# Performance work log

Measured on AMD Instinct MI355X. Metric: run time of the kernel, lower is better.

## Reference

```python
import jax, jax.numpy as jnp
import numpy as np

TOPK = 4          # config.top_prob_values
NBINS = 32        # config.max_num_bins -> bins per corner = NBINS+1 = 33
HID = 64          # config.lqe_hidden_dim
B, L = 64, 4096


def setup_inputs() -> dict:
    key = jax.random.key(0)
    k1, k2, k3, k4 = jax.random.split(key, 4)
    in_dim = 4 * (TOPK + 1)  # 20
    scores = jax.random.normal(k1, (B, L, 1), dtype=jnp.float32)
    pred_corners = jax.random.normal(k2, (B, L, 4 * (NBINS + 1)), dtype=jnp.float32)
    # Deimv2MLP (DFineMLP) with num_layers=2: Linear(20,64) -> relu -> Linear(64,1)
    w1 = jax.random.normal(k3, (in_dim, HID), dtype=jnp.float32) / np.sqrt(in_dim)
    b1 = jnp.zeros((HID,), dtype=jnp.float32)
    w2 = jax.random.normal(k4, (HID, 1), dtype=jnp.float32) / np.sqrt(HID)
    b2 = jnp.zeros((1,), dtype=jnp.float32)
    return {"scores": scores, "pred_corners": pred_corners,
            "w1": w1, "b1": b1, "w2": w2, "b2": b2}


def reference(scores, pred_corners, w1, b1, w2, b2):
    b, l, _ = pred_corners.shape
    # softmax over bins per corner: (B, L, 4, NBINS+1)
    prob = jax.nn.softmax(pred_corners.reshape(b, l, 4, NBINS + 1), axis=-1)
    prob_topk, _ = jax.lax.top_k(prob, TOPK)                     # (B, L, 4, TOPK)
    stat = jnp.concatenate([prob_topk,
                            prob_topk.mean(axis=-1, keepdims=True)], axis=-1)
    stat = stat.reshape(b, l, 4 * (TOPK + 1))                    # (B, L, 20)
    h = jax.nn.relu(stat @ w1 + b1)                              # (B, L, 64)
    quality_score = h @ w2 + b2                                  # (B, L, 1)
    return scores + quality_score
```

## Files before the change

kernel.cpp:

```cpp
#include <hip/hip_runtime.h>


#define THREADS 256
#define ROWS 64

typedef float f32x4 __attribute__((ext_vector_type(4), aligned(16)));

__device__ __forceinline__ void sort4d(float& a, float& b, float& c, float& d) {
    float t;
    t = fmaxf(a, b); b = fminf(a, b); a = t;
    t = fmaxf(c, d); d = fminf(c, d); c = t;
    t = fmaxf(a, c); c = fminf(a, c); a = t;
    t = fmaxf(b, d); d = fminf(b, d); b = t;
    t = fmaxf(b, c); c = fminf(b, c); b = t;
}
__device__ __forceinline__ void ins4(float& a, float& b, float& c, float& d,
                                     float x) {
    float t;
    t = fmaxf(a, x); x = fminf(a, x); a = t;
    t = fmaxf(b, x); x = fminf(b, x); b = t;
    t = fmaxf(c, x); x = fminf(c, x); c = t;
    d = fmaxf(d, x);
}
__device__ __forceinline__ void merge4(float& a0, float& a1, float& a2,
                                       float& a3, float b0, float b1,
                                       float b2, float b3) {
    a0 = fmaxf(a0, b3);
    a1 = fmaxf(a1, b2);
    a2 = fmaxf(a2, b1);
    a3 = fmaxf(a3, b0);
    sort4d(a0, a1, a2, a3);
}

__global__ __launch_bounds__(THREADS, 4)
void lqe_kernel(const float* __restrict__ scores,
                const float* __restrict__ pc,
                const float* __restrict__ w1,
                const float* __restrict__ b1,
                const float* __restrict__ w2,
                const float* __restrict__ b2,
                float* __restrict__ out)
{
    __shared__ float smStage[ROWS * 132];

    const int t  = threadIdx.x;
    const int wv = t >> 6;
    const int l  = t & 63;
    const long long rowBase = (long long)blockIdx.x * ROWS;

    float sc = 0.f;
    if (t < 64) sc = scores[rowBase + t];

    {
        const f32x4* __restrict__ src =
            (const f32x4*)(pc + rowBase * 132) + wv * 528;
        f32x4* dst = (f32x4*)smStage + wv * 528;
        #pragma unroll
        for (int i = 0; i < 8; ++i) dst[l + i * 64] = src[l + i * 64];
        if (l < 16) dst[512 + l] = src[512 + l];
    }

    {
        const float* v = smStage + wv * 2112 + l * 33;
        float x[33];
        #pragma unroll
        for (int k = 0; k < 33; ++k) x[k] = v[k];

        float a0 = x[0],  a1 = x[1],  a2 = x[2],  a3 = x[3];
        float c0 = x[8],  c1 = x[9],  c2 = x[10], c3 = x[11];
        float d0 = x[16], d1 = x[17], d2 = x[18], d3 = x[19];
        float e0 = x[24], e1 = x[25], e2 = x[26], e3 = x[27];
        sort4d(a0, a1, a2, a3);
        sort4d(c0, c1, c2, c3);
        sort4d(d0, d1, d2, d3);
        sort4d(e0, e1, e2, e3);
        #pragma unroll
        for (int k = 0; k < 4; ++k) {
            ins4(a0, a1, a2, a3, x[4 + k]);
            ins4(c0, c1, c2, c3, x[12 + k]);
            ins4(d0, d1, d2, d3, x[20 + k]);
            ins4(e0, e1, e2, e3, x[28 + k]);
        }
        ins4(e0, e1, e2, e3, x[32]);
        merge4(a0, a1, a2, a3, c0, c1, c2, c3);
        merge4(d0, d1, d2, d3, e0, e1, e2, e3);
        merge4(a0, a1, a2, a3, d0, d1, d2, d3);
        const float t0 = a0, t1 = a1, t2 = a2, t3 = a3;

        float sa = 0.f, sb = 0.f, scc = 0.f, sd = 0.f;
        #pragma unroll
        for (int k = 0; k < 32; k += 4) {
            sa  += __expf(x[k + 0] - t0);
            sb  += __expf(x[k + 1] - t0);
            scc += __expf(x[k + 2] - t0);
            sd  += __expf(x[k + 3] - t0);
        }
        sa += __expf(x[32] - t0);
        const float inv = 1.0f / ((sa + sb) + (scc + sd));
        const float p0 = inv;
        const float p1 = __expf(t1 - t0) * inv;
        const float p2 = __expf(t2 - t0) * inv;
        const float p3 = __expf(t3 - t0) * inv;
        const float pm = 0.25f * (p0 + p1 + p2 + p3);

        float* sd_ = smStage + wv * 2112 + (l >> 2) * 21 + (l & 3) * 5;
        sd_[0] = p0; sd_[1] = p1; sd_[2] = p2; sd_[3] = p3; sd_[4] = pm;
    }
    __syncthreads();

    {
        const int wvs = __builtin_amdgcn_readfirstlane(wv);
        const float* __restrict__ w1s = w1 + wvs * 16;
        const float* __restrict__ w2s = w2 + wvs * 16;
        const float* __restrict__ b1s = b1 + wvs * 16;

        float st[20];
        #pragma unroll
        for (int k = 0; k < 20; ++k)
            st[k] = smStage[(l >> 4) * 2112 + (l & 15) * 21 + k];

        float h[16];
        #pragma unroll
        for (int j = 0; j < 16; ++j) h[j] = b1s[j];
        #pragma unroll
        for (int k = 0; k < 20; ++k) {
            #pragma unroll
            for (int j = 0; j < 16; ++j)
                h[j] = fmaf(st[k], w1s[k * 64 + j], h[j]);
        }
        float acc0 = 0.f, acc1 = 0.f, acc2 = 0.f, acc3 = 0.f;
        #pragma unroll
        for (int j = 0; j < 16; j += 4) {
            acc0 = fmaf(fmaxf(h[j + 0], 0.f), w2s[j + 0], acc0);
            acc1 = fmaf(fmaxf(h[j + 1], 0.f), w2s[j + 1], acc1);
            acc2 = fmaf(fmaxf(h[j + 2], 0.f), w2s[j + 2], acc2);
            acc3 = fmaf(fmaxf(h[j + 3], 0.f), w2s[j + 3], acc3);
        }
        smStage[wvs * 2112 + 400 + l] = (acc0 + acc1) + (acc2 + acc3);
    }
    __syncthreads();

    if (t < 64) {
        const float r = (smStage[400 + t]        + smStage[2112 + 400 + t]) +
                        (smStage[4224 + 400 + t] + smStage[6336 + 400 + t]);
        out[rowBase + t] = sc + r + b2[0];
    }
}

extern "C" void kernel_launch(void* const* d_in, const int* in_sizes, int n_in,
                              void* d_out, int out_size, void* d_ws, size_t ws_size,
                              hipStream_t stream) {
    const float* scores = (const float*)d_in[0];
    const float* pc     = (const float*)d_in[1];
    const float* w1     = (const float*)d_in[2];
    const float* b1     = (const float*)d_in[3];
    const float* w2     = (const float*)d_in[4];
    const float* b2     = (const float*)d_in[5];
    float* out = (float*)d_out;

    const int rows = out_size;
    const int blocks = rows / ROWS;
    lqe_kernel<<<blocks, THREADS, 0, stream>>>(scores, pc, w1, b1, w2, b2, out);
}
```

Before: 33.72 us.

## Process 128 rows per block with both global loads issued before compute

```diff
diff --git a/kernel.cpp b/kernel.cpp
--- a/kernel.cpp
+++ b/kernel.cpp
@@ -2,7 +2,7 @@
 
 
 #define THREADS 256
-#define ROWS 64
+#define BLOCK_ROWS 128
 
 typedef float f32x4 __attribute__((ext_vector_type(4), aligned(16)));
 
@@ -32,7 +32,7 @@
     sort4d(a0, a1, a2, a3);
 }
 
-__global__ __launch_bounds__(THREADS, 4)
+__global__ __launch_bounds__(THREADS, 2)
 void lqe_kernel(const float* __restrict__ scores,
                 const float* __restrict__ pc,
                 const float* __restrict__ w1,
@@ -41,27 +41,33 @@
                 const float* __restrict__ b2,
                 float* __restrict__ out)
 {
-    __shared__ float smStage[ROWS * 132];
+    __shared__ float smStage[BLOCK_ROWS * 132];
 
     const int t  = threadIdx.x;
     const int wv = t >> 6;
     const int l  = t & 63;
-    const long long rowBase = (long long)blockIdx.x * ROWS;
+    const long long rowBase = (long long)blockIdx.x * BLOCK_ROWS;
 
     float sc = 0.f;
-    if (t < 64) sc = scores[rowBase + t];
+    if (t < BLOCK_ROWS) sc = scores[rowBase + t];
 
-    {
+    const int g0 = 2 * wv, g1 = 2 * wv + 1;
+
+    auto load_g = [&](int g, f32x4 (&r)[8], f32x4& tl) {
         const f32x4* __restrict__ src =
-            (const f32x4*)(pc + rowBase * 132) + wv * 528;
-        f32x4* dst = (f32x4*)smStage + wv * 528;
+            (const f32x4*)(pc + (rowBase + (long long)g * 16) * 132);
         #pragma unroll
-        for (int i = 0; i < 8; ++i) dst[l + i * 64] = src[l + i * 64];
-        if (l < 16) dst[512 + l] = src[512 + l];
-    }
-
-    {
-        const float* v = smStage + wv * 2112 + l * 33;
+        for (int i = 0; i < 8; ++i) r[i] = src[l + i * 64];
+        if (l < 16) tl = src[512 + l];
+    };
+    auto write_g = [&](int g, const f32x4 (&r)[8], const f32x4& tl) {
+        f32x4* dst = (f32x4*)smStage + g * 528;
+        #pragma unroll
+        for (int i = 0; i < 8; ++i) dst[l + i * 64] = r[i];
+        if (l < 16) dst[512 + l] = tl;
+    };
+    auto corner_g = [&](int g) {
+        const float* v = smStage + g * 2112 + l * 33;
         float x[33];
         #pragma unroll
         for (int k = 0; k < 33; ++k) x[k] = v[k];
@@ -103,9 +109,17 @@
         const float p3 = __expf(t3 - t0) * inv;
         const float pm = 0.25f * (p0 + p1 + p2 + p3);
 
-        float* sd_ = smStage + wv * 2112 + (l >> 2) * 21 + (l & 3) * 5;
+        float* sd_ = smStage + g * 2112 + (l >> 2) * 21 + (l & 3) * 5;
         sd_[0] = p0; sd_[1] = p1; sd_[2] = p2; sd_[3] = p3; sd_[4] = pm;
-    }
+    };
+
+    f32x4 ra[8], rb[8], ta, tb;
+    load_g(g0, ra, ta);
+    load_g(g1, rb, tb);
+    write_g(g0, ra, ta);
+    corner_g(g0);
+    write_g(g1, rb, tb);
+    corner_g(g1);
     __syncthreads();
 
     {
@@ -114,35 +128,39 @@
         const float* __restrict__ w2s = w2 + wvs * 16;
         const float* __restrict__ b1s = b1 + wvs * 16;
 
-        float st[20];
         #pragma unroll
-        for (int k = 0; k < 20; ++k)
-            st[k] = smStage[(l >> 4) * 2112 + (l & 15) * 21 + k];
+        for (int half = 0; half < 2; ++half) {
+            const int r = half * 64 + l;
+            float st[20];
+            #pragma unroll
+            for (int k = 0; k < 20; ++k)
+                st[k] = smStage[(r >> 4) * 2112 + (r & 15) * 21 + k];
 
-        float h[16];
-        #pragma unroll
-        for (int j = 0; j < 16; ++j) h[j] = b1s[j];
-        #pragma unroll
-        for (int k = 0; k < 20; ++k) {
+            float h[16];
             #pragma unroll
-            for (int j = 0; j < 16; ++j)
-                h[j] = fmaf(st[k], w1s[k * 64 + j], h[j]);
+            for (int j = 0; j < 16; ++j) h[j] = b1s[j];
+            #pragma unroll
+            for (int k = 0; k < 20; ++k) {
+                #pragma unroll
+                for (int j = 0; j < 16; ++j)
+                    h[j] = fmaf(st[k], w1s[k * 64 + j], h[j]);
+            }
+            float acc0 = 0.f, acc1 = 0.f, acc2 = 0.f, acc3 = 0.f;
+            #pragma unroll
+            for (int j = 0; j < 16; j += 4) {
+                acc0 = fmaf(fmaxf(h[j + 0], 0.f), w2s[j + 0], acc0);
+                acc1 = fmaf(fmaxf(h[j + 1], 0.f), w2s[j + 1], acc1);
+                acc2 = fmaf(fmaxf(h[j + 2], 0.f), w2s[j + 2], acc2);
+                acc3 = fmaf(fmaxf(h[j + 3], 0.f), w2s[j + 3], acc3);
+            }
+            smStage[wvs * 4224 + 400 + r] = (acc0 + acc1) + (acc2 + acc3);
         }
-        float acc0 = 0.f, acc1 = 0.f, acc2 = 0.f, acc3 = 0.f;
-        #pragma unroll
-        for (int j = 0; j < 16; j += 4) {
-            acc0 = fmaf(fmaxf(h[j + 0], 0.f), w2s[j + 0], acc0);
-            acc1 = fmaf(fmaxf(h[j + 1], 0.f), w2s[j + 1], acc1);
-            acc2 = fmaf(fmaxf(h[j + 2], 0.f), w2s[j + 2], acc2);
-            acc3 = fmaf(fmaxf(h[j + 3], 0.f), w2s[j + 3], acc3);
-        }
-        smStage[wvs * 2112 + 400 + l] = (acc0 + acc1) + (acc2 + acc3);
     }
     __syncthreads();
 
-    if (t < 64) {
-        const float r = (smStage[400 + t]        + smStage[2112 + 400 + t]) +
-                        (smStage[4224 + 400 + t] + smStage[6336 + 400 + t]);
+    if (t < BLOCK_ROWS) {
+        const float r = (smStage[400 + t]        + smStage[4224 + 400 + t]) +
+                        (smStage[8448 + 400 + t] + smStage[12672 + 400 + t]);
         out[rowBase + t] = sc + r + b2[0];
     }
 }
@@ -159,6 +177,6 @@
     float* out = (float*)d_out;
 
     const int rows = out_size;
-    const int blocks = rows / ROWS;
+    const int blocks = rows / BLOCK_ROWS;
     lqe_kernel<<<blocks, THREADS, 0, stream>>>(scores, pc, w1, b1, w2, b2, out);
 }
```

Result: slower. 69.05 us (+104.8%).

## Double-buffer two 64-row tiles per block using direct global-to-LDS loads

Applied to the files above, without the earlier changes.

```diff
diff --git a/kernel.cpp b/kernel.cpp
--- a/kernel.cpp
+++ b/kernel.cpp
@@ -2,9 +2,10 @@
 
 
 #define THREADS 256
-#define ROWS 64
 
 typedef float f32x4 __attribute__((ext_vector_type(4), aligned(16)));
+
+#define BAR_LGKM() asm volatile("s_waitcnt lgkmcnt(0)\n\ts_barrier" ::: "memory")
 
 __device__ __forceinline__ void sort4d(float& a, float& b, float& c, float& d) {
     float t;
@@ -32,7 +33,109 @@
     sort4d(a0, a1, a2, a3);
 }
 
-__global__ __launch_bounds__(THREADS, 4)
+__device__ __forceinline__ void stage_dma(const float* __restrict__ gsrc,
+                                          float (&buf)[8448], int t) {
+    const int wvbase = t & 192;
+    #pragma unroll
+    for (int i = 0; i < 8; ++i)
+        __builtin_amdgcn_global_load_lds(
+            (const __attribute__((address_space(1))) void*)(gsrc + (size_t)(i * 256 + t) * 4),
+            (__attribute__((address_space(3))) void*)(&buf[(i * 256 + wvbase) * 4]),
+            16, 0, 0);
+    if (t < 64)
+        __builtin_amdgcn_global_load_lds(
+            (const __attribute__((address_space(1))) void*)(gsrc + (size_t)(2048 + t) * 4),
+            (__attribute__((address_space(3))) void*)(&buf[2048 * 4]),
+            16, 0, 0);
+}
+
+__device__ __forceinline__ void corner_tile(float (&buf)[8448], int t) {
+    const float* v = &buf[t * 33];
+    float x[33];
+    #pragma unroll
+    for (int k = 0; k < 33; ++k) x[k] = v[k];
+
+    float a0 = x[0],  a1 = x[1],  a2 = x[2],  a3 = x[3];
+    float c0 = x[8],  c1 = x[9],  c2 = x[10], c3 = x[11];
+    float d0 = x[16], d1 = x[17], d2 = x[18], d3 = x[19];
+    float e0 = x[24], e1 = x[25], e2 = x[26], e3 = x[27];
+    sort4d(a0, a1, a2, a3);
+    sort4d(c0, c1, c2, c3);
+    sort4d(d0, d1, d2, d3);
+    sort4d(e0, e1, e2, e3);
+    #pragma unroll
+    for (int k = 0; k < 4; ++k) {
+        ins4(a0, a1, a2, a3, x[4 + k]);
+        ins4(c0, c1, c2, c3, x[12 + k]);
+        ins4(d0, d1, d2, d3, x[20 + k]);
+        ins4(e0, e1, e2, e3, x[28 + k]);
+    }
+    ins4(e0, e1, e2, e3, x[32]);
+    merge4(a0, a1, a2, a3, c0, c1, c2, c3);
+    merge4(d0, d1, d2, d3, e0, e1, e2, e3);
+    merge4(a0, a1, a2, a3, d0, d1, d2, d3);
+    const float t0 = a0, t1 = a1, t2 = a2, t3 = a3;
+
+    float sa = 0.f, sb = 0.f, scc = 0.f, sd = 0.f;
+    #pragma unroll
+    for (int k = 0; k < 32; k += 4) {
+        sa  += __expf(x[k + 0] - t0);
+        sb  += __expf(x[k + 1] - t0);
+        scc += __expf(x[k + 2] - t0);
+        sd  += __expf(x[k + 3] - t0);
+    }
+    sa += __expf(x[32] - t0);
+    const float inv = 1.0f / ((sa + sb) + (scc + sd));
+    const float p0 = inv;
+    const float p1 = __expf(t1 - t0) * inv;
+    const float p2 = __expf(t2 - t0) * inv;
+    const float p3 = __expf(t3 - t0) * inv;
+    const float pm = 0.25f * (p0 + p1 + p2 + p3);
+
+    float* sd_ = &buf[(t & 192) * 33 + ((t >> 2) & 15) * 21 + (t & 3) * 5];
+    sd_[0] = p0; sd_[1] = p1; sd_[2] = p2; sd_[3] = p3; sd_[4] = pm;
+}
+
+__device__ __forceinline__ void mlp_tile(float (&buf)[8448], int t,
+                                         const float* __restrict__ w1,
+                                         const float* __restrict__ b1,
+                                         const float* __restrict__ w2) {
+    const int l = t & 63;
+    const int wvs = __builtin_amdgcn_readfirstlane(t >> 6);
+    const float* __restrict__ w1s = w1 + wvs * 16;
+    const float* __restrict__ w2s = w2 + wvs * 16;
+    const float* __restrict__ b1s = b1 + wvs * 16;
+
+    float st[20];
+    #pragma unroll
+    for (int k = 0; k < 20; ++k)
+        st[k] = buf[(l >> 4) * 2112 + (l & 15) * 21 + k];
+
+    float h[16];
+    #pragma unroll
+    for (int j = 0; j < 16; ++j) h[j] = b1s[j];
+    #pragma unroll
+    for (int k = 0; k < 20; ++k) {
+        #pragma unroll
+        for (int j = 0; j < 16; ++j)
+            h[j] = fmaf(st[k], w1s[k * 64 + j], h[j]);
+    }
+    float acc0 = 0.f, acc1 = 0.f, acc2 = 0.f, acc3 = 0.f;
+    #pragma unroll
+    for (int j = 0; j < 16; j += 4) {
+        acc0 = fmaf(fmaxf(h[j + 0], 0.f), w2s[j + 0], acc0);
+        acc1 = fmaf(fmaxf(h[j + 1], 0.f), w2s[j + 1], acc1);
+        acc2 = fmaf(fmaxf(h[j + 2], 0.f), w2s[j + 2], acc2);
+        acc3 = fmaf(fmaxf(h[j + 3], 0.f), w2s[j + 3], acc3);
+    }
+    buf[wvs * 2112 + 400 + l] = (acc0 + acc1) + (acc2 + acc3);
+}
+
+__device__ __forceinline__ float reduce4(float (&buf)[8448], int t) {
+    return (buf[400 + t] + buf[2512 + t]) + (buf[4624 + t] + buf[6736 + t]);
+}
+
+__global__ __launch_bounds__(THREADS, 2)
 void lqe_kernel(const float* __restrict__ scores,
                 const float* __restrict__ pc,
                 const float* __restrict__ w1,
@@ -41,110 +144,36 @@
                 const float* __restrict__ b2,
                 float* __restrict__ out)
 {
-    __shared__ float smStage[ROWS * 132];
+    __shared__ float smA[8448];
+    __shared__ float smB[8448];
 
-    const int t  = threadIdx.x;
-    const int wv = t >> 6;
-    const int l  = t & 63;
-    const long long rowBase = (long long)blockIdx.x * ROWS;
+    const int t = threadIdx.x;
+    const long long blockRow0 = (long long)blockIdx.x * 128;
+    const float b2v = b2[0];
 
-    float sc = 0.f;
-    if (t < 64) sc = scores[rowBase + t];
-
-    {
-        const f32x4* __restrict__ src =
-            (const f32x4*)(pc + rowBase * 132) + wv * 528;
-        f32x4* dst = (f32x4*)smStage + wv * 528;
-        #pragma unroll
-        for (int i = 0; i < 8; ++i) dst[l + i * 64] = src[l + i * 64];
-        if (l < 16) dst[512 + l] = src[512 + l];
+    float sc0 = 0.f, sc1 = 0.f;
+    if (t < 64) {
+        sc0 = scores[blockRow0 + t];
+        sc1 = scores[blockRow0 + 64 + t];
     }
 
-    {
-        const float* v = smStage + wv * 2112 + l * 33;
-        float x[33];
-        #pragma unroll
-        for (int k = 0; k < 33; ++k) x[k] = v[k];
-
-        float a0 = x[0],  a1 = x[1],  a2 = x[2],  a3 = x[3];
-        float c0 = x[8],  c1 = x[9],  c2 = x[10], c3 = x[11];
-        float d0 = x[16], d1 = x[17], d2 = x[18], d3 = x[19];
-        float e0 = x[24], e1 = x[25], e2 = x[26], e3 = x[27];
-        sort4d(a0, a1, a2, a3);
-        sort4d(c0, c1, c2, c3);
-        sort4d(d0, d1, d2, d3);
-        sort4d(e0, e1, e2, e3);
-        #pragma unroll
-        for (int k = 0; k < 4; ++k) {
-            ins4(a0, a1, a2, a3, x[4 + k]);
-            ins4(c0, c1, c2, c3, x[12 + k]);
-            ins4(d0, d1, d2, d3, x[20 + k]);
-            ins4(e0, e1, e2, e3, x[28 + k]);
-        }
-        ins4(e0, e1, e2, e3, x[32]);
-        merge4(a0, a1, a2, a3, c0, c1, c2, c3);
-        merge4(d0, d1, d2, d3, e0, e1, e2, e3);
-        merge4(a0, a1, a2, a3, d0, d1, d2, d3);
-        const float t0 = a0, t1 = a1, t2 = a2, t3 = a3;
-
-        float sa = 0.f, sb = 0.f, scc = 0.f, sd = 0.f;
-        #pragma unroll
-        for (int k = 0; k < 32; k += 4) {
-            sa  += __expf(x[k + 0] - t0);
-            sb  += __expf(x[k + 1] - t0);
-            scc += __expf(x[k + 2] - t0);
-            sd  += __expf(x[k + 3] - t0);
-        }
-        sa += __expf(x[32] - t0);
-        const float inv = 1.0f / ((sa + sb) + (scc + sd));
-        const float p0 = inv;
-        const float p1 = __expf(t1 - t0) * inv;
-        const float p2 = __expf(t2 - t0) * inv;
-        const float p3 = __expf(t3 - t0) * inv;
-        const float pm = 0.25f * (p0 + p1 + p2 + p3);
-
-        float* sd_ = smStage + wv * 2112 + (l >> 2) * 21 + (l & 3) * 5;
-        sd_[0] = p0; sd_[1] = p1; sd_[2] = p2; sd_[3] = p3; sd_[4] = pm;
-    }
+    stage_dma(pc + blockRow0 * 132, smA, t);
     __syncthreads();
 
-    {
-        const int wvs = __builtin_amdgcn_readfirstlane(wv);
-        const float* __restrict__ w1s = w1 + wvs * 16;
-        const float* __restrict__ w2s = w2 + wvs * 16;
-        const float* __restrict__ b1s = b1 + wvs * 16;
-
-        float st[20];
-        #pragma unroll
-        for (int k = 0; k < 20; ++k)
-            st[k] = smStage[(l >> 4) * 2112 + (l & 15) * 21 + k];
-
-        float h[16];
-        #pragma unroll
-        for (int j = 0; j < 16; ++j) h[j] = b1s[j];
-        #pragma unroll
-        for (int k = 0; k < 20; ++k) {
-            #pragma unroll
-            for (int j = 0; j < 16; ++j)
-                h[j] = fmaf(st[k], w1s[k * 64 + j], h[j]);
-        }
-        float acc0 = 0.f, acc1 = 0.f, acc2 = 0.f, acc3 = 0.f;
-        #pragma unroll
-        for (int j = 0; j < 16; j += 4) {
-            acc0 = fmaf(fmaxf(h[j + 0], 0.f), w2s[j + 0], acc0);
-            acc1 = fmaf(fmaxf(h[j + 1], 0.f), w2s[j + 1], acc1);
-            acc2 = fmaf(fmaxf(h[j + 2], 0.f), w2s[j + 2], acc2);
-            acc3 = fmaf(fmaxf(h[j + 3], 0.f), w2s[j + 3], acc3);
-        }
-        smStage[wvs * 2112 + 400 + l] = (acc0 + acc1) + (acc2 + acc3);
-    }
+    stage_dma(pc + (blockRow0 + 64) * 132, smB, t);
+    __builtin_amdgcn_sched_barrier(0);
+    corner_tile(smA, t);
+    BAR_LGKM();
+    mlp_tile(smA, t, w1, b1, w2);
+    BAR_LGKM();
+    if (t < 64) out[blockRow0 + t] = sc0 + reduce4(smA, t) + b2v;
     __syncthreads();
 
-    if (t < 64) {
-        const float r = (smStage[400 + t]        + smStage[2112 + 400 + t]) +
-                        (smStage[4224 + 400 + t] + smStage[6336 + 400 + t]);
-        out[rowBase + t] = sc + r + b2[0];
-    }
+    corner_tile(smB, t);
+    BAR_LGKM();
+    mlp_tile(smB, t, w1, b1, w2);
+    BAR_LGKM();
+    if (t < 64) out[blockRow0 + 64 + t] = sc1 + reduce4(smB, t) + b2v;
 }
 
 extern "C" void kernel_launch(void* const* d_in, const int* in_sizes, int n_in,
@@ -159,6 +188,6 @@
     float* out = (float*)d_out;
 
     const int rows = out_size;
-    const int blocks = rows / ROWS;
+    const int blocks = rows / 128;
     lqe_kernel<<<blocks, THREADS, 0, stream>>>(scores, pc, w1, b1, w2, b2, out);
 }
```

New measurement: 39.68 us. 17.7% more time.

## Split each corner across two lanes and halve rows per block

Applied to the files above, without the earlier changes.

```diff
diff --git a/kernel.cpp b/kernel.cpp
--- a/kernel.cpp
+++ b/kernel.cpp
@@ -2,7 +2,7 @@
 
 
 #define THREADS 256
-#define ROWS 64
+#define ROWS 32
 
 typedef float f32x4 __attribute__((ext_vector_type(4), aligned(16)));
 
@@ -32,7 +32,7 @@
     sort4d(a0, a1, a2, a3);
 }
 
-__global__ __launch_bounds__(THREADS, 4)
+__global__ __launch_bounds__(THREADS, 8)
 void lqe_kernel(const float* __restrict__ scores,
                 const float* __restrict__ pc,
                 const float* __restrict__ w1,
@@ -41,7 +41,9 @@
                 const float* __restrict__ b2,
                 float* __restrict__ out)
 {
-    __shared__ float smStage[ROWS * 132];
+    __shared__ f32x4 smStage4[ROWS * 33];
+    __shared__ float smPart[128];
+    float* const smStage = (float*)smStage4;
 
     const int t  = threadIdx.x;
     const int wv = t >> 6;
@@ -49,66 +51,66 @@
     const long long rowBase = (long long)blockIdx.x * ROWS;
 
     float sc = 0.f;
-    if (t < 64) sc = scores[rowBase + t];
+    if (t < ROWS) sc = scores[rowBase + t];
 
     {
-        const f32x4* __restrict__ src =
-            (const f32x4*)(pc + rowBase * 132) + wv * 528;
-        f32x4* dst = (f32x4*)smStage + wv * 528;
+        const f32x4* __restrict__ src = (const f32x4*)(pc + rowBase * 132);
         #pragma unroll
-        for (int i = 0; i < 8; ++i) dst[l + i * 64] = src[l + i * 64];
-        if (l < 16) dst[512 + l] = src[512 + l];
-    }
-
-    {
-        const float* v = smStage + wv * 2112 + l * 33;
-        float x[33];
-        #pragma unroll
-        for (int k = 0; k < 33; ++k) x[k] = v[k];
-
-        float a0 = x[0],  a1 = x[1],  a2 = x[2],  a3 = x[3];
-        float c0 = x[8],  c1 = x[9],  c2 = x[10], c3 = x[11];
-        float d0 = x[16], d1 = x[17], d2 = x[18], d3 = x[19];
-        float e0 = x[24], e1 = x[25], e2 = x[26], e3 = x[27];
-        sort4d(a0, a1, a2, a3);
-        sort4d(c0, c1, c2, c3);
-        sort4d(d0, d1, d2, d3);
-        sort4d(e0, e1, e2, e3);
-        #pragma unroll
-        for (int k = 0; k < 4; ++k) {
-            ins4(a0, a1, a2, a3, x[4 + k]);
-            ins4(c0, c1, c2, c3, x[12 + k]);
-            ins4(d0, d1, d2, d3, x[20 + k]);
-            ins4(e0, e1, e2, e3, x[28 + k]);
-        }
-        ins4(e0, e1, e2, e3, x[32]);
-        merge4(a0, a1, a2, a3, c0, c1, c2, c3);
-        merge4(d0, d1, d2, d3, e0, e1, e2, e3);
-        merge4(a0, a1, a2, a3, d0, d1, d2, d3);
-        const float t0 = a0, t1 = a1, t2 = a2, t3 = a3;
-
-        float sa = 0.f, sb = 0.f, scc = 0.f, sd = 0.f;
-        #pragma unroll
-        for (int k = 0; k < 32; k += 4) {
-            sa  += __expf(x[k + 0] - t0);
-            sb  += __expf(x[k + 1] - t0);
-            scc += __expf(x[k + 2] - t0);
-            sd  += __expf(x[k + 3] - t0);
-        }
-        sa += __expf(x[32] - t0);
-        const float inv = 1.0f / ((sa + sb) + (scc + sd));
-        const float p0 = inv;
-        const float p1 = __expf(t1 - t0) * inv;
-        const float p2 = __expf(t2 - t0) * inv;
-        const float p3 = __expf(t3 - t0) * inv;
-        const float pm = 0.25f * (p0 + p1 + p2 + p3);
-
-        float* sd_ = smStage + wv * 2112 + (l >> 2) * 21 + (l & 3) * 5;
-        sd_[0] = p0; sd_[1] = p1; sd_[2] = p2; sd_[3] = p3; sd_[4] = pm;
+        for (int i = 0; i < 4; ++i) smStage4[t + i * 256] = src[t + i * 256];
+        if (t < 32) smStage4[1024 + t] = src[1024 + t];
     }
     __syncthreads();
 
     {
+        const int half = t & 1;
+        const float* v =
+            smStage + (t >> 3) * 132 + ((t >> 1) & 3) * 33 + half * 16;
+        float x[17];
+        #pragma unroll
+        for (int k = 0; k < 17; ++k) x[k] = v[k];
+        if (half) x[0] = -3.0e38f;
+
+        float a0 = x[0], a1 = x[1], a2 = x[2], a3 = x[3];
+        sort4d(a0, a1, a2, a3);
+        #pragma unroll
+        for (int k = 4; k < 17; ++k) ins4(a0, a1, a2, a3, x[k]);
+
+        float sa = 0.f, sb = 0.f, sg = 0.f, sd = 0.f;
+        #pragma unroll
+        for (int k = 0; k < 16; k += 4) {
+            sa += __expf(x[k + 0] - a0);
+            sb += __expf(x[k + 1] - a0);
+            sg += __expf(x[k + 2] - a0);
+            sd += __expf(x[k + 3] - a0);
+        }
+        sa += __expf(x[16] - a0);
+        const float s = (sa + sb) + (sg + sd);
+
+        const float o0 = __shfl_xor(a0, 1);
+        const float o1 = __shfl_xor(a1, 1);
+        const float o2 = __shfl_xor(a2, 1);
+        const float o3 = __shfl_xor(a3, 1);
+        const float os = __shfl_xor(s, 1);
+
+        float T0 = a0, T1 = a1, T2 = a2, T3 = a3;
+        merge4(T0, T1, T2, T3, o0, o1, o2, o3);
+        const float S = s * __expf(a0 - T0) + os * __expf(o0 - T0);
+        const float inv = 1.0f / S;
+        const float p0 = inv;
+        const float p1 = __expf(T1 - T0) * inv;
+        const float p2 = __expf(T2 - T0) * inv;
+        const float p3 = __expf(T3 - T0) * inv;
+        const float pm = 0.25f * (p0 + p1 + p2 + p3);
+
+        if (!half) {
+            float* sd_ = smStage + wv * 1056 + ((t >> 3) & 7) * 21 +
+                         ((t >> 1) & 3) * 5;
+            sd_[0] = p0; sd_[1] = p1; sd_[2] = p2; sd_[3] = p3; sd_[4] = pm;
+        }
+    }
+    __syncthreads();
+
+    if (l < 32) {
         const int wvs = __builtin_amdgcn_readfirstlane(wv);
         const float* __restrict__ w1s = w1 + wvs * 16;
         const float* __restrict__ w2s = w2 + wvs * 16;
@@ -117,7 +119,7 @@
         float st[20];
         #pragma unroll
         for (int k = 0; k < 20; ++k)
-            st[k] = smStage[(l >> 4) * 2112 + (l & 15) * 21 + k];
+            st[k] = smStage[(l >> 3) * 1056 + (l & 7) * 21 + k];
 
         float h[16];
         #pragma unroll
@@ -136,13 +138,13 @@
             acc2 = fmaf(fmaxf(h[j + 2], 0.f), w2s[j + 2], acc2);
             acc3 = fmaf(fmaxf(h[j + 3], 0.f), w2s[j + 3], acc3);
         }
-        smStage[wvs * 2112 + 400 + l] = (acc0 + acc1) + (acc2 + acc3);
+        smPart[wvs * 32 + l] = (acc0 + acc1) + (acc2 + acc3);
     }
     __syncthreads();
 
-    if (t < 64) {
-        const float r = (smStage[400 + t]        + smStage[2112 + 400 + t]) +
-                        (smStage[4224 + 400 + t] + smStage[6336 + 400 + t]);
+    if (t < ROWS) {
+        const float r = (smPart[t] + smPart[32 + t]) +
+                        (smPart[64 + t] + smPart[96 + t]);
         out[rowBase + t] = sc + r + b2[0];
     }
 }
```

After: 37.77 us. 1.12x slower.
